# Performance work log

Measured on AMD Instinct MI355X. Metric: run time of the kernel, lower is better.

Reference implementation:

```python
import jax, jax.numpy as jnp
import numpy as np

N, E, DIN, GB, GD, LB, LD, G = 50000, 640000, 64, 128, 4, 256, 2, 1024


def setup_inputs() -> dict:
    key = jax.random.key(0)
    ks = jax.random.split(key, 20)
    p = lambda k, shape: (jax.random.normal(k, shape, dtype=jnp.float32) * 0.05)
    return {
        "x": jax.random.normal(ks[0], (N, DIN), dtype=jnp.float32),
        "edge_index": jax.random.randint(ks[1], (2, E), 0, N, dtype=jnp.int64),
        "batch": jnp.sort(jax.random.randint(ks[2], (N,), 0, G, dtype=jnp.int64)),
        "num_graphs": G,
        "W0": p(ks[3], (DIN, GB)), "b0": p(ks[4], (GB,)),
        "Wg": p(ks[5], (GD, GB, GB)), "bg": p(ks[6], (GD, GB)),
        "gamma_g": jnp.ones((GD, GB), jnp.float32), "beta_g": jnp.zeros((GD, GB), jnp.float32),
        "Wl0": p(ks[7], (GB, LB)), "bl0": p(ks[8], (LB,)),
        "Wl": p(ks[9], (LD, LB, LB)), "bl": p(ks[10], (LD, LB)),
        "gamma_l": jnp.ones((LD, LB), jnp.float32), "beta_l": jnp.zeros((LD, LB), jnp.float32),
        "Wout": p(ks[11], (LB, 2)), "bout": p(ks[12], (2,)),
    }


def reference(x, edge_index, batch, num_graphs, W0, b0, Wg, bg, gamma_g, beta_g,
              Wl0, bl0, Wl, bl, gamma_l, beta_l, Wout, bout):
    n = x.shape[0]
    src, dst = edge_index[0], edge_index[1]
    # GCN degree normalization with self loops: deg = 1 + in-degree
    deg = jax.ops.segment_sum(jnp.ones(src.shape[0], x.dtype), dst, num_segments=n) + 1.0
    dinv = jax.lax.rsqrt(deg)                 # deg^{-1/2}
    enorm = dinv[src] * dinv[dst]             # [E] edge norm
    snorm = dinv * dinv                       # [N] self-loop norm (deg^{-1})

    def gcn(h, W, b):
        hw = h @ W                                            # [N, GB]
        agg = jax.ops.segment_sum(hw[src] * enorm[:, None], dst, num_segments=n)
        return agg + hw * snorm[:, None] + b

    def bn(h, g, bt):  # training-mode batchnorm (biased var), eps=1e-5
        m = h.mean(0)
        v = h.var(0)
        return (h - m) * jax.lax.rsqrt(v + 1e-5) * g + bt

    h = jax.nn.relu(gcn(x, W0, b0))
    for i in range(Wg.shape[0]):
        h = jax.nn.relu(bn(gcn(h, Wg[i], bg[i]), gamma_g[i], beta_g[i]))
    # global_add_pool
    hp = jax.ops.segment_sum(h, batch, num_segments=num_graphs)  # [G, GB]
    h = jax.nn.relu(hp @ Wl0 + bl0)
    for i in range(Wl.shape[0]):
        h = jax.nn.relu(bn(h @ Wl[i] + bl[i], gamma_l[i], beta_l[i]))
    return h @ Wout + bout
```

## Files before the change

### kernel.cpp

```cpp
#include <hip/hip_runtime.h>

#define NN 50000
#define EE 640000
#define DINv 64
#define GBv 128
#define GDv 4
#define LBv 256
#define LDv 2
#define GGv 1024

#define NB 196
#define BCAP 4096
#define BTILE 4096
#define NBT ((EE + BTILE - 1) / BTILE)

#define NTILES ((NN + 63) / 64)
#define UPN (NN * 16)
#define CONVN (DINv * GBv + GDv * GBv * GBv)

typedef _Float16 f16x8 __attribute__((ext_vector_type(8)));
typedef float f32x4 __attribute__((ext_vector_type(4)));

__device__ __forceinline__ float h2f(ushort u) {
  union { ushort u; _Float16 h; } x;
  x.u = u;
  return (float)x.h;
}
__device__ __forceinline__ ushort f2h(float f) {
  union { ushort u; _Float16 h; } x;
  x.h = (_Float16)f;
  return x.u;
}


__global__ __launch_bounds__(256) void k_bucket(const int* __restrict__ ei,
                                                int* __restrict__ bcnt,
                                                uint* __restrict__ bkt) {
  __shared__ int lcnt[NB];
  __shared__ int lbase[NB];
  __shared__ int gbase[NB];
  __shared__ int ls[256];
  __shared__ uint stage[BTILE];
  __shared__ ushort sb[BTILE];
  int tid = threadIdx.x;
  int t0 = blockIdx.x * BTILE;
  int cnt = min(BTILE, EE - t0);
  for (int i = tid; i < NB; i += 256) lcnt[i] = 0;
  __syncthreads();

  uint en[16];
  int bb[16], rk[16];
  int nper = (cnt + 255) >> 8;
  for (int k = 0; k < nper; k++) {
    int e = k * 256 + tid;
    if (e < cnt) {
      int src = ei[t0 + e];
      int dst = ei[EE + t0 + e];
      int b = dst >> 8;
      en[k] = ((uint)src << 8) | (uint)(dst & 255);
      bb[k] = b;
      rk[k] = atomicAdd(&lcnt[b], 1);
    } else {
      bb[k] = -1;
    }
  }
  __syncthreads();

  int v = (tid < NB) ? lcnt[tid] : 0;
  ls[tid] = v;
  __syncthreads();
  for (int off = 1; off < 256; off <<= 1) {
    int t = (tid >= off) ? ls[tid - off] : 0;
    __syncthreads();
    ls[tid] += t;
    __syncthreads();
  }
  if (tid < NB) {
    lbase[tid] = ls[tid] - v;
    gbase[tid] = atomicAdd(&bcnt[tid], v);
  }
  __syncthreads();

  for (int k = 0; k < nper; k++) {
    if (bb[k] >= 0) {
      int slot = lbase[bb[k]] + rk[k];
      stage[slot] = en[k];
      sb[slot] = (ushort)bb[k];
    }
  }
  __syncthreads();

  for (int i = tid; i < cnt; i += 256) {
    int b = sb[i];
    bkt[(size_t)b * BCAP + gbase[b] + (i - lbase[b])] = stage[i];
  }
}


__global__ __launch_bounds__(256) void k_csr(const uint* __restrict__ bkt,
                                             const int* __restrict__ bcnt,
                                             int* __restrict__ offs,
                                             float* __restrict__ dinv,
                                             int* __restrict__ col,
                                             int* __restrict__ deg,
                                             int* __restrict__ ghist) {
  __shared__ int lhist[256];
  __shared__ int lofs[256];
  __shared__ int lcur[256];
  __shared__ int lsb[256];
  __shared__ int lh2[64];
  int b = blockIdx.x;
  int tid = threadIdx.x;
  int bv = (tid < NB) ? bcnt[tid] : 0;
  lsb[tid] = bv;
  lhist[tid] = 0;
  if (tid < 64) lh2[tid] = 0;
  __syncthreads();
  for (int off = 1; off < 256; off <<= 1) {
    int t = (tid >= off) ? lsb[tid - off] : 0;
    __syncthreads();
    lsb[tid] += t;
    __syncthreads();
  }
  int cnt = bcnt[b];
  int base = lsb[b] - cnt;
  const uint* B = bkt + (size_t)b * BCAP;
  for (int i = tid; i < cnt; i += 256) atomicAdd(&lhist[B[i] & 255], 1);
  __syncthreads();
  int v = lhist[tid];
  lofs[tid] = v;
  __syncthreads();
  for (int off = 1; off < 256; off <<= 1) {
    int t = (tid >= off) ? lofs[tid - off] : 0;
    __syncthreads();
    lofs[tid] += t;
    __syncthreads();
  }
  int excl = lofs[tid] - v;
  int n = b * 256 + tid;
  if (n < NN) {
    offs[n] = base + excl;
    dinv[n] = rsqrtf((float)(v + 1));
    int d = min(v, 63);
    deg[n] = d;
    atomicAdd(&lh2[d], 1);
  }
  lcur[tid] = excl;
  __syncthreads();
  if (tid < 64 && lh2[tid]) atomicAdd(&ghist[tid], lh2[tid]);
  if (b == 0 && tid == 0) offs[NN] = EE;
  for (int i = tid; i < cnt; i += 256) {
    uint e = B[i];
    int p = atomicAdd(&lcur[e & 255], 1);
    col[base + p] = (int)(e >> 8);
  }
}


__global__ __launch_bounds__(256) void k_dperm(const int* __restrict__ deg,
                                               const int* __restrict__ ghist,
                                               int* __restrict__ gcur,
                                               int* __restrict__ perm) {
  __shared__ int lhist[64];
  __shared__ int lbase[64];
  int tid = threadIdx.x;
  if (tid < 64) lhist[tid] = 0;
  __syncthreads();
  int n = blockIdx.x * 256 + tid;
  int d = 0, rk = 0;
  if (n < NN) {
    d = deg[n];
    rk = atomicAdd(&lhist[d], 1);
  }
  __syncthreads();
  if (tid < 64) {
    int s = 0;
    for (int i = tid + 1; i < 64; i++) s += ghist[i];
    if (lhist[tid]) lbase[tid] = s + atomicAdd(&gcur[tid], lhist[tid]);
  }
  __syncthreads();
  if (n < NN) perm[lbase[d] + rk] = n;
}


__global__ __launch_bounds__(256) void k_prep(const float* __restrict__ x,
                                              const float* __restrict__ dinv,
                                              const float* __restrict__ W0,
                                              const float* __restrict__ Wg,
                                              ushort* __restrict__ u,
                                              ushort* __restrict__ Wt0,
                                              ushort* __restrict__ Wtg) {
  int idx = blockIdx.x * 256 + threadIdx.x;
  if (idx < UPN) {
    int n = idx >> 4;
    float4 v = ((const float4*)x)[idx];
    float d = dinv[n];
    union { ushort us[4]; uint2 q; } o;
    o.us[0] = f2h(v.x * d);
    o.us[1] = f2h(v.y * d);
    o.us[2] = f2h(v.z * d);
    o.us[3] = f2h(v.w * d);
    ((uint2*)u)[idx] = o.q;
  } else {
    int j = idx - UPN;
    if (j < DINv * GBv) {
      int c = j >> 6, k = j & 63;
      Wt0[j] = f2h(W0[k * GBv + c]);
    } else if (j < CONVN) {
      int e = j - DINv * GBv;
      int i = e >> 14, rem = e & 16383;
      int c = rem >> 7, k = rem & 127;
      Wtg[e] = f2h(Wg[i * GBv * GBv + k * GBv + c]);
    }
  }
}


template <int K, int MODE, bool STATS>
__global__ __launch_bounds__(256) void k_layer(const ushort* __restrict__ Gin,
                                               const int* __restrict__ col,
                                               const int* __restrict__ offs,
                                               const float* __restrict__ dinv,
                                               const int* __restrict__ perm,
                                               const float* __restrict__ st,
                                               const float* __restrict__ gamma,
                                               const float* __restrict__ beta,
                                               const ushort* __restrict__ Wt,
                                               const float* __restrict__ bias,
                                               float* __restrict__ stG,
                                               ushort* __restrict__ Gout) {
  constexpr int VEC = K / 16;
  constexpr int KP = K + 8;
  constexpr int CP = 136;
  constexpr bool REUSE = (K == 128);
  __shared__ __attribute__((aligned(16))) _Float16 sW[128 * KP];
  __shared__ __attribute__((aligned(16))) _Float16 sA[64 * KP];
  __shared__ __attribute__((aligned(16))) _Float16 sCbuf[REUSE ? 8 : 64 * CP];
  __shared__ float sB[128], sS[128], sT[128];
  __shared__ float ssum[128], ssq[128];
  _Float16* sC = REUSE ? sA : sCbuf;
  int tid = threadIdx.x;

  {
    constexpr int CH = K / 8;
    for (int i = tid; i < 128 * CH; i += 256) {
      int c = i / CH, ch = i - c * CH;
      *(uint4*)&sW[c * KP + ch * 8] = ((const uint4*)Wt)[i];
    }
  }
  if (tid < 128) {
    sB[tid] = bias[tid];
    if constexpr (STATS) {
      ssum[tid] = 0.f;
      ssq[tid] = 0.f;
    }
    if constexpr (MODE == 2) {
      float mu = st[tid] * (1.f / NN);
      float var = st[128 + tid] * (1.f / NN) - mu * mu;
      float s = rsqrtf(var + 1e-5f) * gamma[tid];
      sS[tid] = s;
      sT[tid] = beta[tid] - mu * s;
    }
  }
  if constexpr (MODE == 2) __syncthreads();

  int w = tid >> 6, lane = tid & 63;
  int quad = lane >> 4, m = lane & 15;
  int row0 = blockIdx.x * 64;

  float sc[VEC], tc[VEC];
  if constexpr (MODE == 2) {
#pragma unroll
    for (int v = 0; v < VEC; v++) {
      sc[v] = sS[m * VEC + v];
      tc[v] = sT[m * VEC + v];
    }
  }

  union U { uint4 v4; uint2 v2; ushort us[8]; };
  auto loadrow = [&](int s) {
    U u;
    const ushort* p = Gin + (long)s * K + m * VEC;
    if constexpr (VEC == 8) u.v4 = *(const uint4*)p;
    else u.v2 = *(const uint2*)p;
    return u;
  };

  for (int rnd = 0; rnd < 4; rnd++) {
    int r = rnd * 16 + w * 4 + quad;
    int idx = row0 + r;
    float acc[VEC];
#pragma unroll
    for (int v = 0; v < VEC; v++) acc[v] = 0.f;
    float dn = 0.f;
    if (idx < NN) {
      int n = perm[idx];
      dn = dinv[n];
      auto addrow = [&](U u, float dv) {
#pragma unroll
        for (int v = 0; v < VEC; v++) {
          float g = h2f(u.us[v]);
          if constexpr (MODE == 0) acc[v] += g;
          else if constexpr (MODE == 1) acc[v] += fmaxf(g, 0.f) * dv;
          else acc[v] += fmaxf(g * sc[v] + tc[v], 0.f) * dv;
        }
      };
      addrow(loadrow(n), dn);
      int s0 = offs[n], s1 = offs[n + 1];
      int j = s0;
      for (; j + 7 < s1; j += 8) {
        int si[8];
#pragma unroll
        for (int t = 0; t < 8; t++) si[t] = col[j + t];
        U uu[8];
#pragma unroll
        for (int t = 0; t < 8; t++) uu[t] = loadrow(si[t]);
        float dd[8];
#pragma unroll
        for (int t = 0; t < 8; t++) dd[t] = (MODE != 0) ? dinv[si[t]] : 0.f;
#pragma unroll
        for (int t = 0; t < 8; t++) addrow(uu[t], dd[t]);
      }
      for (; j + 3 < s1; j += 4) {
        int si[4];
#pragma unroll
        for (int t = 0; t < 4; t++) si[t] = col[j + t];
        U uu[4];
#pragma unroll
        for (int t = 0; t < 4; t++) uu[t] = loadrow(si[t]);
        float dd[4];
#pragma unroll
        for (int t = 0; t < 4; t++) dd[t] = (MODE != 0) ? dinv[si[t]] : 0.f;
#pragma unroll
        for (int t = 0; t < 4; t++) addrow(uu[t], dd[t]);
      }
      for (; j < s1; j++) {
        int s = col[j];
        U u = loadrow(s);
        float dv = (MODE != 0) ? dinv[s] : 0.f;
        addrow(u, dv);
      }
    }
    U o;
#pragma unroll
    for (int v = 0; v < VEC; v++) o.us[v] = f2h(acc[v] * dn);
    _Float16* ap = &sA[r * KP + m * VEC];
    if constexpr (VEC == 8) *(uint4*)ap = o.v4;
    else *(uint2*)ap = o.v2;
  }
  __syncthreads();

  f32x4 acc2[8];
#pragma unroll
  for (int ct = 0; ct < 8; ct++) acc2[ct] = (f32x4){0.f, 0.f, 0.f, 0.f};
  const _Float16* pa = &sA[(16 * w + m) * KP + quad * 8];
#pragma unroll
  for (int ks = 0; ks < K; ks += 32) {
    f16x8 a = *(const f16x8*)(pa + ks);
#pragma unroll
    for (int ct = 0; ct < 8; ct++) {
      f16x8 bfr = *(const f16x8*)&sW[(ct * 16 + m) * KP + ks + quad * 8];
      acc2[ct] = __builtin_amdgcn_mfma_f32_16x16x32_f16(a, bfr, acc2[ct], 0, 0, 0);
    }
  }

  int crow = 16 * w + quad * 4;
  float ps[8], pq[8];
  if constexpr (STATS) {
#pragma unroll
    for (int ct = 0; ct < 8; ct++) {
      int c = ct * 16 + m;
      float bb = sB[c];
      ps[ct] = 0.f;
      pq[ct] = 0.f;
#pragma unroll
      for (int r = 0; r < 4; r++) {
        if (row0 + crow + r < NN) {
          float g = acc2[ct][r] + bb;
          ps[ct] += g;
          pq[ct] += g * g;
        }
      }
    }
  }
  if constexpr (REUSE) __syncthreads();

#pragma unroll
  for (int ct = 0; ct < 8; ct++) {
    int c = ct * 16 + m;
    float bb = sB[c];
#pragma unroll
    for (int r = 0; r < 4; r++) sC[(crow + r) * CP + c] = (_Float16)(acc2[ct][r] + bb);
  }
  __syncthreads();

  {
    int r = tid >> 2, col0 = (tid & 3) * 32;
    int idx = row0 + r;
    if (idx < NN) {
      int node = perm[idx];
      const uint4* srcp = (const uint4*)&sC[r * CP + col0];
      uint4* dst = (uint4*)(Gout + (long)node * 128 + col0);
#pragma unroll
      for (int ch = 0; ch < 4; ch++) dst[ch] = srcp[ch];
    }
  }

  if constexpr (STATS) {
#pragma unroll
    for (int ct = 0; ct < 8; ct++) {
      float s = ps[ct], q = pq[ct];
      s += __shfl_xor(s, 16);
      q += __shfl_xor(q, 16);
      s += __shfl_xor(s, 32);
      q += __shfl_xor(q, 32);
      if (quad == 0) {
        atomicAdd(&ssum[ct * 16 + m], s);
        atomicAdd(&ssq[ct * 16 + m], q);
      }
    }
    __syncthreads();
    if (tid < 128) {
      int c = (tid + blockIdx.x * 8) & 127;
      atomicAdd(&stG[c], ssum[c]);
      atomicAdd(&stG[128 + c], ssq[c]);
    }
  }
}


__global__ __launch_bounds__(128) void k_pool2(const ushort* __restrict__ G,
                                               const float* __restrict__ st,
                                               const float* __restrict__ gamma,
                                               const float* __restrict__ beta,
                                               const int* __restrict__ batch,
                                               float* __restrict__ hp) {
  __shared__ int sse[2];
  int g = blockIdx.x;
  int c = threadIdx.x;
  if (c < 2) {
    int key = g + c;
    int lo = 0, hi = NN;
    while (lo < hi) {
      int mid = (lo + hi) >> 1;
      if (batch[mid] < key) lo = mid + 1;
      else hi = mid;
    }
    sse[c] = lo;
  }
  __syncthreads();
  int s = sse[0], e = sse[1];
  float m = st[c] * (1.f / NN);
  float v = st[128 + c] * (1.f / NN) - m * m;
  float sc = rsqrtf(v + 1e-5f) * gamma[c];
  float tc = beta[c] - m * sc;
  float acc = 0.f;
  for (int n = s; n < e; n++) acc += fmaxf(h2f(G[(long)n * 128 + c]) * sc + tc, 0.f);
  hp[(long)g * 128 + c] = acc;
}


__global__ void k_colstats(const float* __restrict__ X, int rows, float* __restrict__ st) {
  int c = threadIdx.x;
  int C = blockDim.x;
  float s = 0.f, q = 0.f;
  for (int r = blockIdx.x; r < rows; r += gridDim.x) {
    float v = X[(long)r * C + c];
    s += v;
    q += v * v;
  }
  atomicAdd(&st[c], s);
  atomicAdd(&st[C + c], q);
}


template <int KIN, int MODE>
__global__ __launch_bounds__(256) void k_fc(const float* __restrict__ X,
                                            const float* __restrict__ W,
                                            const float* __restrict__ b,
                                            const float* __restrict__ st,
                                            const float* __restrict__ gamma,
                                            const float* __restrict__ beta,
                                            float* __restrict__ Y) {
  __shared__ float sx[KIN];
  int g = blockIdx.x;
  int c = threadIdx.x;
  for (int k = c; k < KIN; k += 256) {
    float v = X[(long)g * KIN + k];
    if constexpr (MODE == 2) {
      float m = st[k] * (1.f / GGv);
      float var = st[KIN + k] * (1.f / GGv) - m * m;
      v = fmaxf((v - m) * rsqrtf(var + 1e-5f) * gamma[k] + beta[k], 0.f);
    }
    sx[k] = v;
  }
  __syncthreads();
  float acc = b[c];
#pragma unroll 8
  for (int k = 0; k < KIN; k++) acc += sx[k] * W[(long)k * 256 + c];
  Y[(long)g * 256 + c] = (MODE == 0) ? fmaxf(acc, 0.f) : acc;
}

__global__ __launch_bounds__(256) void k_out(const float* __restrict__ X,
                                             const float* __restrict__ st,
                                             const float* __restrict__ gamma,
                                             const float* __restrict__ beta,
                                             const float* __restrict__ Wout,
                                             const float* __restrict__ bout,
                                             float* __restrict__ out) {
  int g = blockIdx.x * 4 + (threadIdx.x >> 6);
  int l = threadIdx.x & 63;
  float a0 = 0.f, a1 = 0.f;
  for (int k = l; k < LBv; k += 64) {
    float z = X[(long)g * LBv + k];
    float m = st[k] * (1.f / GGv);
    float var = st[LBv + k] * (1.f / GGv) - m * m;
    float x = fmaxf((z - m) * rsqrtf(var + 1e-5f) * gamma[k] + beta[k], 0.f);
    a0 += x * Wout[2 * k];
    a1 += x * Wout[2 * k + 1];
  }
  for (int off = 32; off > 0; off >>= 1) {
    a0 += __shfl_down(a0, off);
    a1 += __shfl_down(a1, off);
  }
  if (l == 0) {
    out[2 * g] = a0 + bout[0];
    out[2 * g + 1] = a1 + bout[1];
  }
}


extern "C" void kernel_launch(void* const* d_in, const int* in_sizes, int n_in,
                              void* d_out, int out_size, void* d_ws, size_t ws_size,
                              hipStream_t stream) {
  const float* x = (const float*)d_in[0];
  const int* ei = (const int*)d_in[1];
  const int* batch = (const int*)d_in[2];
  const float* W0 = (const float*)d_in[4];
  const float* b0 = (const float*)d_in[5];
  const float* Wg = (const float*)d_in[6];
  const float* bg = (const float*)d_in[7];
  const float* gamma_g = (const float*)d_in[8];
  const float* beta_g = (const float*)d_in[9];
  const float* Wl0 = (const float*)d_in[10];
  const float* bl0 = (const float*)d_in[11];
  const float* Wl = (const float*)d_in[12];
  const float* bl = (const float*)d_in[13];
  const float* gamma_l = (const float*)d_in[14];
  const float* beta_l = (const float*)d_in[15];
  const float* Wout = (const float*)d_in[16];
  const float* bout = (const float*)d_in[17];
  float* out = (float*)d_out;

  char* w = (char*)d_ws;
  auto alloc = [&](size_t bytes) {
    void* p = (void*)w;
    w += (bytes + 255) & ~(size_t)255;
    return p;
  };
  int* bcnt = (int*)alloc((size_t)NB * 4);
  float* stAll = (float*)alloc((size_t)(4 * 256 + 2 * 512) * 4);
  int* ghist = (int*)alloc((size_t)64 * 4);
  int* gcur = (int*)alloc((size_t)64 * 4);
  size_t zspan = (char*)w - (char*)bcnt;
  uint* bkt = (uint*)alloc((size_t)NB * BCAP * 4);
  int* offs = (int*)alloc((size_t)(NN + 1) * 4);
  int* col = (int*)alloc((size_t)EE * 4);
  float* dinv = (float*)alloc((size_t)NN * 4);
  int* deg = (int*)alloc((size_t)NN * 4);
  int* perm = (int*)alloc((size_t)NN * 4);
  ushort* u = (ushort*)alloc((size_t)NN * DINv * 2);
  ushort* g1 = (ushort*)alloc((size_t)NN * GBv * 2);
  ushort* g2 = (ushort*)alloc((size_t)NN * GBv * 2);
  ushort* Wt0 = (ushort*)alloc((size_t)DINv * GBv * 2);
  ushort* Wtg = (ushort*)alloc((size_t)GDv * GBv * GBv * 2);
  float* hp = (float*)alloc((size_t)GGv * GBv * 4);
  float* m1 = (float*)alloc((size_t)GGv * LBv * 4);
  float* m2 = (float*)alloc((size_t)GGv * LBv * 4);

  float* stg = stAll;
  float* sth0 = stAll + 4 * 256;
  float* sth1 = sth0 + 512;

  hipMemsetAsync(bcnt, 0, zspan, stream);

  k_bucket<<<NBT, 256, 0, stream>>>(ei, bcnt, bkt);
  k_csr<<<NB, 256, 0, stream>>>(bkt, bcnt, offs, dinv, col, deg, ghist);
  k_dperm<<<NB, 256, 0, stream>>>(deg, ghist, gcur, perm);
  k_prep<<<(UPN + CONVN + 255) / 256, 256, 0, stream>>>(x, dinv, W0, Wg, u, Wt0, Wtg);

  k_layer<64, 0, false><<<NTILES, 256, 0, stream>>>(u, col, offs, dinv, perm, nullptr,
                                                    nullptr, nullptr, Wt0, b0, nullptr, g1);
  k_layer<128, 1, true><<<NTILES, 256, 0, stream>>>(g1, col, offs, dinv, perm, nullptr,
                                                    nullptr, nullptr, Wtg, bg, stg, g2);
  for (int i = 1; i < GDv; i++) {
    const ushort* gin = (i & 1) ? g2 : g1;
    ushort* gout = (i & 1) ? g1 : g2;
    k_layer<128, 2, true><<<NTILES, 256, 0, stream>>>(
        gin, col, offs, dinv, perm, stg + (size_t)(i - 1) * 256,
        gamma_g + (size_t)(i - 1) * GBv, beta_g + (size_t)(i - 1) * GBv,
        Wtg + (size_t)i * GBv * GBv, bg + (size_t)i * GBv, stg + (size_t)i * 256, gout);
  }

  k_pool2<<<GGv, 128, 0, stream>>>(g1, stg + 3 * 256, gamma_g + 3 * GBv, beta_g + 3 * GBv,
                                   batch, hp);

  k_fc<GBv, 0><<<GGv, 256, 0, stream>>>(hp, Wl0, bl0, nullptr, nullptr, nullptr, m1);
  k_fc<LBv, 1><<<GGv, 256, 0, stream>>>(m1, Wl, bl, nullptr, nullptr, nullptr, m2);
  k_colstats<<<256, LBv, 0, stream>>>(m2, GGv, sth0);
  k_fc<LBv, 2><<<GGv, 256, 0, stream>>>(m2, Wl + (size_t)LBv * LBv, bl + LBv, sth0,
                                        gamma_l, beta_l, m1);
  k_colstats<<<256, LBv, 0, stream>>>(m1, GGv, sth1);
  k_out<<<GGv / 4, 256, 0, stream>>>(m1, sth1, gamma_l + LBv, beta_l + LBv, Wout, bout, out);
}
```

Measured before the change: 445.5 us.

## Double k_layer block size, fuse relu-dinv prescale into first layer, branchless gather

Launches the fused aggregate+GEMM layer with 512 threads, so each wave handles fewer aggregation rows and the MFMA output is split into 64-column halves across waves. The first layer now applies ReLU and the dinv scale in its epilogue (OUTF), which lets the second layer use the plain-sum mode without per-edge dinv loads. The neighbor gather loop becomes a single 8-wide loop that clamps indices and zeroes weights on padded lanes, replacing the 8/4/1 remainder loops. k_pool2 is unrolled by four with independent accumulators. In exchange, padded lanes issue redundant loads, and reusing sW as the output staging buffer in the K=64 case adds a barrier.

```diff
diff --git a/kernel.cpp b/kernel.cpp
--- a/kernel.cpp
+++ b/kernel.cpp
@@ -216,34 +216,34 @@
 }
 
 
-template <int K, int MODE, bool STATS>
-__global__ __launch_bounds__(256) void k_layer(const ushort* __restrict__ Gin,
-                                               const int* __restrict__ col,
-                                               const int* __restrict__ offs,
-                                               const float* __restrict__ dinv,
-                                               const int* __restrict__ perm,
-                                               const float* __restrict__ st,
-                                               const float* __restrict__ gamma,
-                                               const float* __restrict__ beta,
-                                               const ushort* __restrict__ Wt,
-                                               const float* __restrict__ bias,
-                                               float* __restrict__ stG,
-                                               ushort* __restrict__ Gout) {
+template <int K, int MODE, bool STATS, bool OUTF>
+__global__ __launch_bounds__(512, 4) void k_layer(const ushort* __restrict__ Gin,
+                                                  const int* __restrict__ col,
+                                                  const int* __restrict__ offs,
+                                                  const float* __restrict__ dinv,
+                                                  const int* __restrict__ perm,
+                                                  const float* __restrict__ st,
+                                                  const float* __restrict__ gamma,
+                                                  const float* __restrict__ beta,
+                                                  const ushort* __restrict__ Wt,
+                                                  const float* __restrict__ bias,
+                                                  float* __restrict__ stG,
+                                                  ushort* __restrict__ Gout) {
   constexpr int VEC = K / 16;
   constexpr int KP = K + 8;
   constexpr int CP = 136;
   constexpr bool REUSE = (K == 128);
   __shared__ __attribute__((aligned(16))) _Float16 sW[128 * KP];
   __shared__ __attribute__((aligned(16))) _Float16 sA[64 * KP];
-  __shared__ __attribute__((aligned(16))) _Float16 sCbuf[REUSE ? 8 : 64 * CP];
   __shared__ float sB[128], sS[128], sT[128];
   __shared__ float ssum[128], ssq[128];
-  _Float16* sC = REUSE ? sA : sCbuf;
+  __shared__ float sDn[64];
+  _Float16* sC = REUSE ? sA : sW;
   int tid = threadIdx.x;
 
   {
     constexpr int CH = K / 8;
-    for (int i = tid; i < 128 * CH; i += 256) {
+    for (int i = tid; i < 128 * CH; i += 512) {
       int c = i / CH, ch = i - c * CH;
       *(uint4*)&sW[c * KP + ch * 8] = ((const uint4*)Wt)[i];
     }
@@ -286,8 +286,8 @@
     return u;
   };
 
-  for (int rnd = 0; rnd < 4; rnd++) {
-    int r = rnd * 16 + w * 4 + quad;
+  for (int rnd = 0; rnd < 2; rnd++) {
+    int r = rnd * 32 + w * 4 + quad;
     int idx = row0 + r;
     float acc[VEC];
 #pragma unroll
@@ -296,50 +296,39 @@
     if (idx < NN) {
       int n = perm[idx];
       dn = dinv[n];
-      auto addrow = [&](U u, float dv) {
+      auto addrow = [&](U u, float wv) {
 #pragma unroll
         for (int v = 0; v < VEC; v++) {
           float g = h2f(u.us[v]);
-          if constexpr (MODE == 0) acc[v] += g;
-          else if constexpr (MODE == 1) acc[v] += fmaxf(g, 0.f) * dv;
-          else acc[v] += fmaxf(g * sc[v] + tc[v], 0.f) * dv;
+          if constexpr (MODE == 2) g = fmaxf(g * sc[v] + tc[v], 0.f);
+          else if constexpr (MODE == 1) g = fmaxf(g, 0.f);
+          acc[v] += g * wv;
         }
       };
-      addrow(loadrow(n), dn);
+      addrow(loadrow(n), (MODE == 0) ? 1.f : dn);
       int s0 = offs[n], s1 = offs[n + 1];
-      int j = s0;
-      for (; j + 7 < s1; j += 8) {
+      for (int j = s0; j < s1; j += 8) {
         int si[8];
 #pragma unroll
-        for (int t = 0; t < 8; t++) si[t] = col[j + t];
+        for (int t = 0; t < 8; t++) {
+          int jj = j + t;
+          si[t] = col[jj < s1 ? jj : s1 - 1];
+        }
         U uu[8];
 #pragma unroll
         for (int t = 0; t < 8; t++) uu[t] = loadrow(si[t]);
-        float dd[8];
-#pragma unroll
-        for (int t = 0; t < 8; t++) dd[t] = (MODE != 0) ? dinv[si[t]] : 0.f;
-#pragma unroll
-        for (int t = 0; t < 8; t++) addrow(uu[t], dd[t]);
+        float wt[8];
+#pragma unroll
+        for (int t = 0; t < 8; t++) {
+          float base = (MODE == 0) ? 1.f : dinv[si[t]];
+          wt[t] = (j + t < s1) ? base : 0.f;
+        }
+#pragma unroll
+        for (int t = 0; t < 8; t++) addrow(uu[t], wt[t]);
       }
-      for (; j + 3 < s1; j += 4) {
-        int si[4];
-#pragma unroll
-        for (int t = 0; t < 4; t++) si[t] = col[j + t];
-        U uu[4];
-#pragma unroll
-        for (int t = 0; t < 4; t++) uu[t] = loadrow(si[t]);
-        float dd[4];
-#pragma unroll
-        for (int t = 0; t < 4; t++) dd[t] = (MODE != 0) ? dinv[si[t]] : 0.f;
-#pragma unroll
-        for (int t = 0; t < 4; t++) addrow(uu[t], dd[t]);
-      }
-      for (; j < s1; j++) {
-        int s = col[j];
-        U u = loadrow(s);
-        float dv = (MODE != 0) ? dinv[s] : 0.f;
-        addrow(u, dv);
-      }
+    }
+    if constexpr (OUTF) {
+      if (m == 0) sDn[r] = dn;
     }
     U o;
 #pragma unroll
@@ -350,26 +339,28 @@
   }
   __syncthreads();
 
-  f32x4 acc2[8];
-#pragma unroll
-  for (int ct = 0; ct < 8; ct++) acc2[ct] = (f32x4){0.f, 0.f, 0.f, 0.f};
-  const _Float16* pa = &sA[(16 * w + m) * KP + quad * 8];
+  int wr = w >> 1, wc = w & 1;
+  f32x4 acc2[4];
+#pragma unroll
+  for (int ct = 0; ct < 4; ct++) acc2[ct] = (f32x4){0.f, 0.f, 0.f, 0.f};
+  const _Float16* pa = &sA[(16 * wr + m) * KP + quad * 8];
 #pragma unroll
   for (int ks = 0; ks < K; ks += 32) {
     f16x8 a = *(const f16x8*)(pa + ks);
 #pragma unroll
-    for (int ct = 0; ct < 8; ct++) {
-      f16x8 bfr = *(const f16x8*)&sW[(ct * 16 + m) * KP + ks + quad * 8];
+    for (int ct = 0; ct < 4; ct++) {
+      int c = wc * 64 + ct * 16 + m;
+      f16x8 bfr = *(const f16x8*)&sW[c * KP + ks + quad * 8];
       acc2[ct] = __builtin_amdgcn_mfma_f32_16x16x32_f16(a, bfr, acc2[ct], 0, 0, 0);
     }
   }
 
-  int crow = 16 * w + quad * 4;
-  float ps[8], pq[8];
+  int crow = 16 * wr + quad * 4;
+  float ps[4], pq[4];
   if constexpr (STATS) {
 #pragma unroll
-    for (int ct = 0; ct < 8; ct++) {
-      int c = ct * 16 + m;
+    for (int ct = 0; ct < 4; ct++) {
+      int c = wc * 64 + ct * 16 + m;
       float bb = sB[c];
       ps[ct] = 0.f;
       pq[ct] = 0.f;
@@ -383,40 +374,50 @@
       }
     }
   }
-  if constexpr (REUSE) __syncthreads();
-
-#pragma unroll
-  for (int ct = 0; ct < 8; ct++) {
-    int c = ct * 16 + m;
+  __syncthreads();
+
+  float dvr[4];
+  if constexpr (OUTF) {
+#pragma unroll
+    for (int r = 0; r < 4; r++) dvr[r] = sDn[crow + r];
+  }
+#pragma unroll
+  for (int ct = 0; ct < 4; ct++) {
+    int c = wc * 64 + ct * 16 + m;
     float bb = sB[c];
 #pragma unroll
-    for (int r = 0; r < 4; r++) sC[(crow + r) * CP + c] = (_Float16)(acc2[ct][r] + bb);
+    for (int r = 0; r < 4; r++) {
+      float y = acc2[ct][r] + bb;
+      if constexpr (OUTF) y = fmaxf(y, 0.f) * dvr[r];
+      sC[(crow + r) * CP + c] = (_Float16)y;
+    }
   }
   __syncthreads();
 
   {
-    int r = tid >> 2, col0 = (tid & 3) * 32;
-    int idx = row0 + r;
-    if (idx < NN) {
-      int node = perm[idx];
-      const uint4* srcp = (const uint4*)&sC[r * CP + col0];
-      uint4* dst = (uint4*)(Gout + (long)node * 128 + col0);
-#pragma unroll
-      for (int ch = 0; ch < 4; ch++) dst[ch] = srcp[ch];
+    int r = tid >> 3;
+    int c0 = (tid & 7) * 16;
+    int idx2 = row0 + r;
+    if (idx2 < NN) {
+      int node = perm[idx2];
+      const uint4* srcp = (const uint4*)&sC[r * CP + c0];
+      uint4* dst = (uint4*)(Gout + (long)node * 128 + c0);
+      dst[0] = srcp[0];
+      dst[1] = srcp[1];
     }
   }
 
   if constexpr (STATS) {
 #pragma unroll
-    for (int ct = 0; ct < 8; ct++) {
+    for (int ct = 0; ct < 4; ct++) {
       float s = ps[ct], q = pq[ct];
       s += __shfl_xor(s, 16);
       q += __shfl_xor(q, 16);
       s += __shfl_xor(s, 32);
       q += __shfl_xor(q, 32);
       if (quad == 0) {
-        atomicAdd(&ssum[ct * 16 + m], s);
-        atomicAdd(&ssq[ct * 16 + m], q);
+        atomicAdd(&ssum[wc * 64 + ct * 16 + m], s);
+        atomicAdd(&ssq[wc * 64 + ct * 16 + m], q);
       }
     }
     __syncthreads();
@@ -454,9 +455,20 @@
   float v = st[128 + c] * (1.f / NN) - m * m;
   float sc = rsqrtf(v + 1e-5f) * gamma[c];
   float tc = beta[c] - m * sc;
-  float acc = 0.f;
-  for (int n = s; n < e; n++) acc += fmaxf(h2f(G[(long)n * 128 + c]) * sc + tc, 0.f);
-  hp[(long)g * 128 + c] = acc;
+  float a0 = 0.f, a1 = 0.f, a2 = 0.f, a3 = 0.f;
+  int n = s;
+  for (; n + 3 < e; n += 4) {
+    float g0 = h2f(G[(long)(n + 0) * 128 + c]);
+    float g1 = h2f(G[(long)(n + 1) * 128 + c]);
+    float g2 = h2f(G[(long)(n + 2) * 128 + c]);
+    float g3 = h2f(G[(long)(n + 3) * 128 + c]);
+    a0 += fmaxf(g0 * sc + tc, 0.f);
+    a1 += fmaxf(g1 * sc + tc, 0.f);
+    a2 += fmaxf(g2 * sc + tc, 0.f);
+    a3 += fmaxf(g3 * sc + tc, 0.f);
+  }
+  for (; n < e; n++) a0 += fmaxf(h2f(G[(long)n * 128 + c]) * sc + tc, 0.f);
+  hp[(long)g * 128 + c] = (a0 + a1) + (a2 + a3);
 }
 
 
@@ -589,14 +601,14 @@
   k_dperm<<<NB, 256, 0, stream>>>(deg, ghist, gcur, perm);
   k_prep<<<(UPN + CONVN + 255) / 256, 256, 0, stream>>>(x, dinv, W0, Wg, u, Wt0, Wtg);
 
-  k_layer<64, 0, false><<<NTILES, 256, 0, stream>>>(u, col, offs, dinv, perm, nullptr,
-                                                    nullptr, nullptr, Wt0, b0, nullptr, g1);
-  k_layer<128, 1, true><<<NTILES, 256, 0, stream>>>(g1, col, offs, dinv, perm, nullptr,
-                                                    nullptr, nullptr, Wtg, bg, stg, g2);
+  k_layer<64, 0, false, true><<<NTILES, 512, 0, stream>>>(
+      u, col, offs, dinv, perm, nullptr, nullptr, nullptr, Wt0, b0, nullptr, g1);
+  k_layer<128, 0, true, false><<<NTILES, 512, 0, stream>>>(
+      g1, col, offs, dinv, perm, nullptr, nullptr, nullptr, Wtg, bg, stg, g2);
   for (int i = 1; i < GDv; i++) {
     const ushort* gin = (i & 1) ? g2 : g1;
     ushort* gout = (i & 1) ? g1 : g2;
-    k_layer<128, 2, true><<<NTILES, 256, 0, stream>>>(
+    k_layer<128, 2, true, false><<<NTILES, 512, 0, stream>>>(
         gin, col, offs, dinv, perm, stg + (size_t)(i - 1) * 256,
         gamma_g + (size_t)(i - 1) * GBv, beta_g + (size_t)(i - 1) * GBv,
         Wtg + (size_t)i * GBv * GBv, bg + (size_t)i * GBv, stg + (size_t)i * 256, gout);
```

Result: faster. 417.2 us (-6.3%).
